# Performance work log

Hardware: AMD Instinct MI355X
Metric: run time of the kernel (lower is better)

Reference implementation:

```python
import jax, jax.numpy as jnp
import numpy as np

BLOCK = 64      # sparse block size (power of 2, >= 16)
NB = 128        # number of blocks -> max_seqlen = 8192
LOCAL = 8       # causal local window, in blocks
GLOBAL = 1      # leading global blocks every query attends to
K = LOCAL + GLOBAL
SM_SCALE = 1.0 / np.sqrt(64.0)  # default sm_scale = 1/sqrt(head_dim)


def _build_layout():
    # Fixed-width equivalent of the CSR block layout: for query block i,
    # live key blocks are the GLOBAL leading blocks plus the LOCAL-wide
    # causal window ending at i. Entries outside [0, i] are masked invalid;
    # global entries that fall inside the local window are invalidated to
    # avoid double counting.
    rows = np.arange(NB)[:, None]
    loc = rows - np.arange(LOCAL - 1, -1, -1)[None, :]      # [NB, LOCAL], ascending, ends at i
    glb = np.tile(np.arange(GLOBAL)[None, :], (NB, 1))      # [NB, GLOBAL]
    loc_valid = loc >= 0
    glb_valid = glb < (rows - LOCAL + 1)                    # strictly below local window
    col = np.concatenate([glb, np.maximum(loc, 0)], axis=1)  # [NB, K]
    valid = np.concatenate([glb_valid, loc_valid], axis=1)   # [NB, K]
    return col.astype(np.int32), valid


def setup_inputs() -> dict:
    key = jax.random.key(0)
    kq, kk, kv = jax.random.split(key, 3)
    B, S, H, D = 2, NB * BLOCK, 16, 64
    q = jax.random.normal(kq, (B, S, H, D), jnp.float32)
    k = jax.random.normal(kk, (B, S, H, D), jnp.float32)
    v = jax.random.normal(kv, (B, S, H, D), jnp.float32)
    col, valid = _build_layout()
    return {"q": q, "k": k, "v": v,
            "col_idx": jnp.asarray(col), "col_valid": jnp.asarray(valid)}


def reference(q, k, v, col_idx, col_valid):
    # Block-sparse causal attention. Only key/value blocks listed in
    # col_idx (where col_valid) are touched; token-level causal mask is
    # applied inside the gathered blocks (diagonal blocks get intra-block
    # causal masking, matching the kernel's behavior).
    B, S, H, D = q.shape
    bs = BLOCK
    nb = S // bs
    qb = q.reshape(B, nb, bs, H, D)                       # [B, nb, bs, H, D]
    kb = k.reshape(B, nb, bs, H, D)[:, col_idx]           # [B, nb, K, bs, H, D]
    vb = v.reshape(B, nb, bs, H, D)[:, col_idx]
    scores = jnp.einsum('bimhd,bijnhd->bhimjn', qb, kb) * SM_SCALE  # [B,H,nb,bs,K,bs]
    qpos = jnp.arange(nb)[:, None] * bs + jnp.arange(bs)[None, :]          # [nb, bs]
    kpos = col_idx[:, :, None] * bs + jnp.arange(bs)[None, None, :]        # [nb, K, bs]
    mask = (kpos[:, None, :, :] <= qpos[:, :, None, None]) & col_valid[:, None, :, None]
    neg = jnp.finfo(scores.dtype).min
    scores = jnp.where(mask[None, None], scores, neg)
    shp = scores.shape
    p = jax.nn.softmax(scores.reshape(shp[0], shp[1], shp[2], shp[3], -1), axis=-1).reshape(shp)
    out = jnp.einsum('bhimjn,bijnhd->bimhd', p, vb)       # [B, nb, bs, H, D]
    return out.reshape(B, S, H, D)
```

## Files before the change

kernel.cpp:

```cpp
#include <hip/hip_runtime.h>
#include <hip/hip_bf16.h>

#define NBQ     128
#define NLOCAL  8
#define NH      16
#define NBATCH  2
#define DIM     64
#define SEQ     (NBQ * 64)
#define QK_SCALE 0.1803368801111204f

typedef __attribute__((ext_vector_type(8))) short bf16x8;
typedef __attribute__((ext_vector_type(4))) short short4v;
typedef __attribute__((ext_vector_type(4))) float f32x4;
typedef __attribute__((ext_vector_type(2))) unsigned int u32x2;

__device__ inline short f2b(float x) {
    unsigned int u = __float_as_uint(x);
    return (short)((u + 0x8000u) >> 16);
}
__device__ inline unsigned int pack2(unsigned int lo_rnd, unsigned int hi_rnd) {
    return __builtin_amdgcn_perm(hi_rnd, lo_rnd, 0x07060302u);
}

typedef union { u32x2 u; short4v s; } pk_u;

__global__ __launch_bounds__(256, 3) void sparse_attn_kernel(
    const float* __restrict__ Q, const float* __restrict__ Kg,
    const float* __restrict__ Vg, float* __restrict__ Out)
{
    __shared__ __align__(16) short sK [64 * 64];
    __shared__ __align__(16) short sVt[64 * 64];

    const int gq  = blockIdx.x >> 5;
    const int bh  = blockIdx.x & 31;
    const int b   = bh >> 4;
    const int h   = bh & 15;
    const int qb0 = gq * 2, qb1 = qb0 + 1;
    const int tid  = threadIdx.x;
    const int wave = tid >> 6;
    const int lane = tid & 63;
    const int quad = lane >> 4;
    const int l15  = lane & 15;

    const int sg   = tid >> 4;
    const int t15c = tid & 15;
    const int tok4 = sg << 2;
    const int ft4  = t15c << 2;

    const int swk = l15 & 7;
    const int swv = ((l15 & 3) << 2) | ((l15 >> 2) & 3);

    bf16x8 qf0[2], qf1[2];
    {
        const int qrow = qb0 * 64 + wave * 16 + l15;
        const float* qp0 = Q + (((size_t)(b * SEQ + qrow)) * NH + h) * DIM;
        const float* qp1 = qp0 + (size_t)64 * NH * DIM;
#pragma unroll
        for (int ks = 0; ks < 2; ++ks) {
            const int o = ks * 32 + quad * 8;
            const f32x4 x0 = *(const f32x4*)(qp0 + o);
            const f32x4 x1 = *(const f32x4*)(qp0 + o + 4);
            const f32x4 y0 = *(const f32x4*)(qp1 + o);
            const f32x4 y1 = *(const f32x4*)(qp1 + o + 4);
            bf16x8 f, g;
#pragma unroll
            for (int c = 0; c < 4; ++c) {
                f[c]     = f2b(x0[c] * QK_SCALE);
                f[c + 4] = f2b(x1[c] * QK_SCALE);
                g[c]     = f2b(y0[c] * QK_SCALE);
                g[c + 4] = f2b(y1[c] * QK_SCALE);
            }
            qf0[ks] = f; qf1[ks] = g;
        }
    }

    float l0 = 0.f, l1 = 0.f;
    f32x4 o0[4], o1[4];
#pragma unroll
    for (int ft = 0; ft < 4; ++ft) { o0[ft] = (f32x4){0,0,0,0}; o1[ft] = (f32x4){0,0,0,0}; }

    const float* kbase = Kg + (size_t)b * (SEQ * NH * DIM);
    const float* vbase = Vg + (size_t)b * (SEQ * NH * DIM);
    const unsigned off0 = (unsigned)((tok4 * NH + h) * DIM + ft4);
    const int NHD = NH * DIM;

    const int lo    = (qb0 - 7 > 0) ? (qb0 - 7) : 0;
    const int has_g = (qb0 >= NLOCAL) ? 1 : 0;
    const int niter = (qb1 - lo + 1) + has_g;

    auto stage_tile = [&](const f32x4 kx[4], const f32x4 vx[4], short* sKb, short* sVb) {
        unsigned int kr[4][4], vr[4][4];
#pragma unroll
        for (int i = 0; i < 4; ++i) {
#pragma unroll
            for (int c = 0; c < 4; ++c) {
                kr[i][c] = __float_as_uint(kx[i][c]) + 0x8000u;
                vr[i][c] = __float_as_uint(vx[i][c]) + 0x8000u;
            }
        }
#pragma unroll
        for (int i = 0; i < 4; ++i) {
            const int row  = tok4 + i;
            const int c16p = ((t15c >> 1) + (row & 7)) & 7;
            u32x2 w;
            w.x = pack2(kr[i][0], kr[i][1]);
            w.y = pack2(kr[i][2], kr[i][3]);
            *(u32x2*)&sKb[row * 64 + c16p * 8 + (t15c & 1) * 4] = w;
        }
#pragma unroll
        for (int c = 0; c < 4; ++c) {
            const int row = ft4 + c;
            const int sig = ((row & 3) << 2) | ((row >> 2) & 3);
            const int ch8 = (sg + sig) & 15;
            u32x2 w;
            w.x = pack2(vr[0][c], vr[1][c]);
            w.y = pack2(vr[2][c], vr[3][c]);
            *(u32x2*)&sVb[row * 64 + ch8 * 4] = w;
        }
    };

    auto compute_tile = [&](const int kb, const short* sKb, const short* sVb) {
        const int a0 = (kb == 0 && qb0 >= NLOCAL) || (kb >= qb0 - 7 && kb <= qb0);
        const int a1 = (kb == 0 && qb1 >= NLOCAL) || (kb >= qb1 - 7);

        f32x4 s0[4], s1[4];
#pragma unroll
        for (int nt = 0; nt < 4; ++nt) {
            const int row = (nt * 16 + l15) * 64;
            const bf16x8 k0 = *(const bf16x8*)&sKb[row + (((quad     + swk) & 7) << 3)];
            const bf16x8 k1 = *(const bf16x8*)&sKb[row + (((4 + quad + swk) & 7) << 3)];
            f32x4 acc0 = (f32x4){0,0,0,0};
            acc0 = __builtin_amdgcn_mfma_f32_16x16x32_bf16(k0, qf0[0], acc0, 0, 0, 0);
            acc0 = __builtin_amdgcn_mfma_f32_16x16x32_bf16(k1, qf0[1], acc0, 0, 0, 0);
            s0[nt] = acc0;
            f32x4 acc1 = (f32x4){0,0,0,0};
            acc1 = __builtin_amdgcn_mfma_f32_16x16x32_bf16(k0, qf1[0], acc1, 0, 0, 0);
            acc1 = __builtin_amdgcn_mfma_f32_16x16x32_bf16(k1, qf1[1], acc1, 0, 0, 0);
            s1[nt] = acc1;
        }

        if (!a0) {
#pragma unroll
            for (int nt = 0; nt < 4; ++nt)
#pragma unroll
                for (int r = 0; r < 4; ++r) s0[nt][r] = -1e30f;
        } else if (kb == qb0) {
            const int qi = wave * 16 + l15;
#pragma unroll
            for (int nt = 0; nt < 4; ++nt)
#pragma unroll
                for (int r = 0; r < 4; ++r)
                    if (nt * 16 + quad * 4 + r > qi) s0[nt][r] = -1e30f;
        }
        if (!a1) {
#pragma unroll
            for (int nt = 0; nt < 4; ++nt)
#pragma unroll
                for (int r = 0; r < 4; ++r) s1[nt][r] = -1e30f;
        } else if (kb == qb1) {
            const int qi = wave * 16 + l15;
#pragma unroll
            for (int nt = 0; nt < 4; ++nt)
#pragma unroll
                for (int r = 0; r < 4; ++r)
                    if (nt * 16 + quad * 4 + r > qi) s1[nt][r] = -1e30f;
        }

        short4v pb0[4], pb1[4];
#pragma unroll
        for (int nt = 0; nt < 4; ++nt) {
            float ps0 = 0.f, ps1 = 0.f;
            unsigned int pr0[4], pr1[4];
#pragma unroll
            for (int r = 0; r < 4; ++r) {
                const float p0 = exp2f(s0[nt][r]);
                const float p1 = exp2f(s1[nt][r]);
                ps0 += p0; ps1 += p1;
                pr0[r] = __float_as_uint(p0) + 0x8000u;
                pr1[r] = __float_as_uint(p1) + 0x8000u;
            }
            l0 += ps0; l1 += ps1;
            pk_u pw0, pw1;
            pw0.u.x = pack2(pr0[0], pr0[1]); pw0.u.y = pack2(pr0[2], pr0[3]);
            pw1.u.x = pack2(pr1[0], pr1[1]); pw1.u.y = pack2(pr1[2], pr1[3]);
            pb0[nt] = pw0.s; pb1[nt] = pw1.s;
        }

#pragma unroll
        for (int ft = 0; ft < 4; ++ft) {
            const int row = (ft * 16 + l15) * 64;
#pragma unroll
            for (int nt = 0; nt < 4; ++nt) {
                const short4v va = *(const short4v*)&sVb[row + (((nt * 4 + quad + swv) & 15) << 2)];
                o0[ft] = __builtin_amdgcn_mfma_f32_16x16x16bf16_1k(va, pb0[nt], o0[ft], 0, 0, 0);
                o1[ft] = __builtin_amdgcn_mfma_f32_16x16x16bf16_1k(va, pb1[nt], o1[ft], 0, 0, 0);
            }
        }
    };

    for (int it = 0; it < niter; ++it) {
        const int kb = (it < has_g) ? 0 : (lo + it - has_g);

        f32x4 kx[4], vx[4];
        const unsigned koff = ((unsigned)kb << 16) + off0;
#pragma unroll
        for (int i = 0; i < 4; ++i) {
            kx[i] = *(const f32x4*)(kbase + koff + i * NHD);
            vx[i] = *(const f32x4*)(vbase + koff + i * NHD);
        }

        __syncthreads();
        stage_tile(kx, vx, &sK[0], &sVt[0]);
        __syncthreads();
        compute_tile(kb, &sK[0], &sVt[0]);
    }

    l0 += __shfl_xor(l0, 16); l0 += __shfl_xor(l0, 32);
    l1 += __shfl_xor(l1, 16); l1 += __shfl_xor(l1, 32);
    const float inv0 = 1.0f / l0;
    const float inv1 = 1.0f / l1;
    const int qrow = qb0 * 64 + wave * 16 + l15;
    float* op0 = Out + (((size_t)(b * SEQ + qrow)) * NH + h) * DIM + quad * 4;
    float* op1 = op0 + (size_t)64 * NH * DIM;
#pragma unroll
    for (int ft = 0; ft < 4; ++ft) {
        *(f32x4*)(op0 + ft * 16) = o0[ft] * inv0;
        *(f32x4*)(op1 + ft * 16) = o1[ft] * inv1;
    }
}

extern "C" void kernel_launch(void* const* d_in, const int* in_sizes, int n_in,
                              void* d_out, int out_size, void* d_ws, size_t ws_size,
                              hipStream_t stream) {
    const float* q = (const float*)d_in[0];
    const float* k = (const float*)d_in[1];
    const float* v = (const float*)d_in[2];
    float* out = (float*)d_out;
    dim3 grid((NBQ / 2) * NBATCH * NH);
    sparse_attn_kernel<<<grid, dim3(256), 0, stream>>>(q, k, v, out);
}
```

Before: 257.9 us.

## Process four query blocks per workgroup and skip MFMAs for inactive key blocks

Each workgroup now handles four consecutive query blocks instead of two, so every staged K/V tile in shared memory is reused by four query blocks and global K/V traffic per query drops. The kernel skips the QK and PV MFMAs for query blocks that do not attend to the current key block, where before it computed them and masked. Float-to-bf16 packing now uses the v_cvt_pk_bf16_f32 instruction instead of an add-and-perm sequence. The grid halves to 1024 workgroups and register use grows with the four accumulator sets, which can lower occupancy and reduce parallelism.

```diff
diff --git a/kernel.cpp b/kernel.cpp
--- a/kernel.cpp
+++ b/kernel.cpp
@@ -18,8 +18,10 @@
     unsigned int u = __float_as_uint(x);
     return (short)((u + 0x8000u) >> 16);
 }
-__device__ inline unsigned int pack2(unsigned int lo_rnd, unsigned int hi_rnd) {
-    return __builtin_amdgcn_perm(hi_rnd, lo_rnd, 0x07060302u);
+__device__ inline unsigned int cvtpk(float lo, float hi) {
+    unsigned int r;
+    asm("v_cvt_pk_bf16_f32 %0, %1, %2" : "=v"(r) : "v"(lo), "v"(hi));
+    return r;
 }
 
 typedef union { u32x2 u; short4v s; } pk_u;
@@ -35,7 +37,7 @@
     const int bh  = blockIdx.x & 31;
     const int b   = bh >> 4;
     const int h   = bh & 15;
-    const int qb0 = gq * 2, qb1 = qb0 + 1;
+    const int qb0 = gq * 4;
     const int tid  = threadIdx.x;
     const int wave = tid >> 6;
     const int lane = tid & 63;
@@ -50,34 +52,32 @@
     const int swk = l15 & 7;
     const int swv = ((l15 & 3) << 2) | ((l15 >> 2) & 3);
 
-    bf16x8 qf0[2], qf1[2];
-    {
-        const int qrow = qb0 * 64 + wave * 16 + l15;
-        const float* qp0 = Q + (((size_t)(b * SEQ + qrow)) * NH + h) * DIM;
-        const float* qp1 = qp0 + (size_t)64 * NH * DIM;
+    bf16x8 qf[4][2];
+#pragma unroll
+    for (int j = 0; j < 4; ++j) {
+        const int qrow = (qb0 + j) * 64 + wave * 16 + l15;
+        const float* qp = Q + (((size_t)(b * SEQ + qrow)) * NH + h) * DIM;
 #pragma unroll
         for (int ks = 0; ks < 2; ++ks) {
             const int o = ks * 32 + quad * 8;
-            const f32x4 x0 = *(const f32x4*)(qp0 + o);
-            const f32x4 x1 = *(const f32x4*)(qp0 + o + 4);
-            const f32x4 y0 = *(const f32x4*)(qp1 + o);
-            const f32x4 y1 = *(const f32x4*)(qp1 + o + 4);
-            bf16x8 f, g;
+            const f32x4 x0 = *(const f32x4*)(qp + o);
+            const f32x4 x1 = *(const f32x4*)(qp + o + 4);
+            bf16x8 f;
 #pragma unroll
             for (int c = 0; c < 4; ++c) {
                 f[c]     = f2b(x0[c] * QK_SCALE);
                 f[c + 4] = f2b(x1[c] * QK_SCALE);
-                g[c]     = f2b(y0[c] * QK_SCALE);
-                g[c + 4] = f2b(y1[c] * QK_SCALE);
             }
-            qf0[ks] = f; qf1[ks] = g;
+            qf[j][ks] = f;
         }
     }
 
-    float l0 = 0.f, l1 = 0.f;
-    f32x4 o0[4], o1[4];
+    float l[4] = {0.f, 0.f, 0.f, 0.f};
+    f32x4 o[4][4];
 #pragma unroll
-    for (int ft = 0; ft < 4; ++ft) { o0[ft] = (f32x4){0,0,0,0}; o1[ft] = (f32x4){0,0,0,0}; }
+    for (int j = 0; j < 4; ++j)
+#pragma unroll
+        for (int ft = 0; ft < 4; ++ft) o[j][ft] = (f32x4){0, 0, 0, 0};
 
     const float* kbase = Kg + (size_t)b * (SEQ * NH * DIM);
     const float* vbase = Vg + (size_t)b * (SEQ * NH * DIM);
@@ -86,120 +86,17 @@
 
     const int lo    = (qb0 - 7 > 0) ? (qb0 - 7) : 0;
     const int has_g = (qb0 >= NLOCAL) ? 1 : 0;
-    const int niter = (qb1 - lo + 1) + has_g;
-
-    auto stage_tile = [&](const f32x4 kx[4], const f32x4 vx[4], short* sKb, short* sVb) {
-        unsigned int kr[4][4], vr[4][4];
-#pragma unroll
-        for (int i = 0; i < 4; ++i) {
-#pragma unroll
-            for (int c = 0; c < 4; ++c) {
-                kr[i][c] = __float_as_uint(kx[i][c]) + 0x8000u;
-                vr[i][c] = __float_as_uint(vx[i][c]) + 0x8000u;
-            }
-        }
-#pragma unroll
-        for (int i = 0; i < 4; ++i) {
-            const int row  = tok4 + i;
-            const int c16p = ((t15c >> 1) + (row & 7)) & 7;
-            u32x2 w;
-            w.x = pack2(kr[i][0], kr[i][1]);
-            w.y = pack2(kr[i][2], kr[i][3]);
-            *(u32x2*)&sKb[row * 64 + c16p * 8 + (t15c & 1) * 4] = w;
-        }
-#pragma unroll
-        for (int c = 0; c < 4; ++c) {
-            const int row = ft4 + c;
-            const int sig = ((row & 3) << 2) | ((row >> 2) & 3);
-            const int ch8 = (sg + sig) & 15;
-            u32x2 w;
-            w.x = pack2(vr[0][c], vr[1][c]);
-            w.y = pack2(vr[2][c], vr[3][c]);
-            *(u32x2*)&sVb[row * 64 + ch8 * 4] = w;
-        }
-    };
-
-    auto compute_tile = [&](const int kb, const short* sKb, const short* sVb) {
-        const int a0 = (kb == 0 && qb0 >= NLOCAL) || (kb >= qb0 - 7 && kb <= qb0);
-        const int a1 = (kb == 0 && qb1 >= NLOCAL) || (kb >= qb1 - 7);
-
-        f32x4 s0[4], s1[4];
-#pragma unroll
-        for (int nt = 0; nt < 4; ++nt) {
-            const int row = (nt * 16 + l15) * 64;
-            const bf16x8 k0 = *(const bf16x8*)&sKb[row + (((quad     + swk) & 7) << 3)];
-            const bf16x8 k1 = *(const bf16x8*)&sKb[row + (((4 + quad + swk) & 7) << 3)];
-            f32x4 acc0 = (f32x4){0,0,0,0};
-            acc0 = __builtin_amdgcn_mfma_f32_16x16x32_bf16(k0, qf0[0], acc0, 0, 0, 0);
-            acc0 = __builtin_amdgcn_mfma_f32_16x16x32_bf16(k1, qf0[1], acc0, 0, 0, 0);
-            s0[nt] = acc0;
-            f32x4 acc1 = (f32x4){0,0,0,0};
-            acc1 = __builtin_amdgcn_mfma_f32_16x16x32_bf16(k0, qf1[0], acc1, 0, 0, 0);
-            acc1 = __builtin_amdgcn_mfma_f32_16x16x32_bf16(k1, qf1[1], acc1, 0, 0, 0);
-            s1[nt] = acc1;
-        }
-
-        if (!a0) {
-#pragma unroll
-            for (int nt = 0; nt < 4; ++nt)
-#pragma unroll
-                for (int r = 0; r < 4; ++r) s0[nt][r] = -1e30f;
-        } else if (kb == qb0) {
-            const int qi = wave * 16 + l15;
-#pragma unroll
-            for (int nt = 0; nt < 4; ++nt)
-#pragma unroll
-                for (int r = 0; r < 4; ++r)
-                    if (nt * 16 + quad * 4 + r > qi) s0[nt][r] = -1e30f;
-        }
-        if (!a1) {
-#pragma unroll
-            for (int nt = 0; nt < 4; ++nt)
-#pragma unroll
-                for (int r = 0; r < 4; ++r) s1[nt][r] = -1e30f;
-        } else if (kb == qb1) {
-            const int qi = wave * 16 + l15;
-#pragma unroll
-            for (int nt = 0; nt < 4; ++nt)
-#pragma unroll
-                for (int r = 0; r < 4; ++r)
-                    if (nt * 16 + quad * 4 + r > qi) s1[nt][r] = -1e30f;
-        }
-
-        short4v pb0[4], pb1[4];
-#pragma unroll
-        for (int nt = 0; nt < 4; ++nt) {
-            float ps0 = 0.f, ps1 = 0.f;
-            unsigned int pr0[4], pr1[4];
-#pragma unroll
-            for (int r = 0; r < 4; ++r) {
-                const float p0 = exp2f(s0[nt][r]);
-                const float p1 = exp2f(s1[nt][r]);
-                ps0 += p0; ps1 += p1;
-                pr0[r] = __float_as_uint(p0) + 0x8000u;
-                pr1[r] = __float_as_uint(p1) + 0x8000u;
-            }
-            l0 += ps0; l1 += ps1;
-            pk_u pw0, pw1;
-            pw0.u.x = pack2(pr0[0], pr0[1]); pw0.u.y = pack2(pr0[2], pr0[3]);
-            pw1.u.x = pack2(pr1[0], pr1[1]); pw1.u.y = pack2(pr1[2], pr1[3]);
-            pb0[nt] = pw0.s; pb1[nt] = pw1.s;
-        }
-
-#pragma unroll
-        for (int ft = 0; ft < 4; ++ft) {
-            const int row = (ft * 16 + l15) * 64;
-#pragma unroll
-            for (int nt = 0; nt < 4; ++nt) {
-                const short4v va = *(const short4v*)&sVb[row + (((nt * 4 + quad + swv) & 15) << 2)];
-                o0[ft] = __builtin_amdgcn_mfma_f32_16x16x16bf16_1k(va, pb0[nt], o0[ft], 0, 0, 0);
-                o1[ft] = __builtin_amdgcn_mfma_f32_16x16x16bf16_1k(va, pb1[nt], o1[ft], 0, 0, 0);
-            }
-        }
-    };
+    const int niter = (qb0 + 3 - lo + 1) + has_g;
 
     for (int it = 0; it < niter; ++it) {
         const int kb = (it < has_g) ? 0 : (lo + it - has_g);
+        bool av[4];
+#pragma unroll
+        for (int j = 0; j < 4; ++j) {
+            const int qbj = qb0 + j;
+            av[j] = (kb == 0 && qb0 >= NLOCAL) || (kb >= qbj - 7 && kb <= qbj);
+        }
+        const int dj = kb - qb0;
 
         f32x4 kx[4], vx[4];
         const unsigned koff = ((unsigned)kb << 16) + off0;
@@ -210,22 +107,80 @@
         }
 
         __syncthreads();
-        stage_tile(kx, vx, &sK[0], &sVt[0]);
+
+#pragma unroll
+        for (int i = 0; i < 4; ++i) {
+            const int row  = tok4 + i;
+            const int c16p = ((t15c >> 1) + (row & 7)) & 7;
+            u32x2 w;
+            w.x = cvtpk(kx[i][0], kx[i][1]);
+            w.y = cvtpk(kx[i][2], kx[i][3]);
+            *(u32x2*)&sK[row * 64 + c16p * 8 + (t15c & 1) * 4] = w;
+        }
+#pragma unroll
+        for (int c = 0; c < 4; ++c) {
+            const int row = ft4 + c;
+            const int sig = ((row & 3) << 2) | ((row >> 2) & 3);
+            const int ch8 = (sg + sig) & 15;
+            u32x2 w;
+            w.x = cvtpk(vx[0][c], vx[1][c]);
+            w.y = cvtpk(vx[2][c], vx[3][c]);
+            *(u32x2*)&sVt[row * 64 + ch8 * 4] = w;
+        }
         __syncthreads();
-        compute_tile(kb, &sK[0], &sVt[0]);
+
+#pragma unroll
+        for (int nt = 0; nt < 4; ++nt) {
+            const int krow = (nt * 16 + l15) * 64;
+            const bf16x8 k0 = *(const bf16x8*)&sK[krow + (((quad     + swk) & 7) << 3)];
+            const bf16x8 k1 = *(const bf16x8*)&sK[krow + (((4 + quad + swk) & 7) << 3)];
+            short4v pbn[4];
+#pragma unroll
+            for (int j = 0; j < 4; ++j) {
+                if (av[j]) {
+                    f32x4 s = (f32x4){0, 0, 0, 0};
+                    s = __builtin_amdgcn_mfma_f32_16x16x32_bf16(k0, qf[j][0], s, 0, 0, 0);
+                    s = __builtin_amdgcn_mfma_f32_16x16x32_bf16(k1, qf[j][1], s, 0, 0, 0);
+                    if (dj == j) {
+                        const int qi = wave * 16 + l15;
+#pragma unroll
+                        for (int r = 0; r < 4; ++r)
+                            if (nt * 16 + quad * 4 + r > qi) s[r] = -1e30f;
+                    }
+                    const float p0 = exp2f(s[0]);
+                    const float p1 = exp2f(s[1]);
+                    const float p2 = exp2f(s[2]);
+                    const float p3 = exp2f(s[3]);
+                    l[j] += (p0 + p1) + (p2 + p3);
+                    pk_u pw;
+                    pw.u.x = cvtpk(p0, p1);
+                    pw.u.y = cvtpk(p2, p3);
+                    pbn[j] = pw.s;
+                }
+            }
+#pragma unroll
+            for (int ft = 0; ft < 4; ++ft) {
+                const short4v va = *(const short4v*)
+                    &sVt[(ft * 16 + l15) * 64 + (((nt * 4 + quad + swv) & 15) << 2)];
+#pragma unroll
+                for (int j = 0; j < 4; ++j)
+                    if (av[j])
+                        o[j][ft] = __builtin_amdgcn_mfma_f32_16x16x16bf16_1k(
+                            va, pbn[j], o[j][ft], 0, 0, 0);
+            }
+        }
     }
 
-    l0 += __shfl_xor(l0, 16); l0 += __shfl_xor(l0, 32);
-    l1 += __shfl_xor(l1, 16); l1 += __shfl_xor(l1, 32);
-    const float inv0 = 1.0f / l0;
-    const float inv1 = 1.0f / l1;
-    const int qrow = qb0 * 64 + wave * 16 + l15;
-    float* op0 = Out + (((size_t)(b * SEQ + qrow)) * NH + h) * DIM + quad * 4;
-    float* op1 = op0 + (size_t)64 * NH * DIM;
 #pragma unroll
-    for (int ft = 0; ft < 4; ++ft) {
-        *(f32x4*)(op0 + ft * 16) = o0[ft] * inv0;
-        *(f32x4*)(op1 + ft * 16) = o1[ft] * inv1;
+    for (int j = 0; j < 4; ++j) {
+        float lj = l[j];
+        lj += __shfl_xor(lj, 16); lj += __shfl_xor(lj, 32);
+        const float inv = 1.0f / lj;
+        const int qrow = (qb0 + j) * 64 + wave * 16 + l15;
+        float* op = Out + (((size_t)(b * SEQ + qrow)) * NH + h) * DIM + quad * 4;
+#pragma unroll
+        for (int ft = 0; ft < 4; ++ft)
+            *(f32x4*)(op + ft * 16) = o[j][ft] * inv;
     }
 }
 
@@ -236,6 +191,6 @@
     const float* k = (const float*)d_in[1];
     const float* v = (const float*)d_in[2];
     float* out = (float*)d_out;
-    dim3 grid((NBQ / 2) * NBATCH * NH);
+    dim3 grid((NBQ / 4) * NBATCH * NH);
     sparse_attn_kernel<<<grid, dim3(256), 0, stream>>>(q, k, v, out);
 }
```

Result: slower. 280.7 us (+8.9%).
